# Kernel optimization log

Measured on AMD Instinct MI355X. Metric: run time of the kernel, lower is better.

The kernel has to match this reference:

```python
import jax, jax.numpy as jnp
import numpy as np

NUM_ROUTING_ITER = 3

def _squash(x):
    # Faithful to torch x.norm(): GLOBAL Frobenius norm over the whole tensor.
    n2 = jnp.sum(x * x)
    return x * (jnp.sqrt(n2) / (1.0 + n2))

def setup_inputs() -> dict:
    key = jax.random.key(0)
    k1, k2 = jax.random.split(key)
    x = jax.random.normal(k1, (256, 1152, 8), dtype=jnp.float32)
    weight = jax.random.normal(k2, (10, 1152, 8, 16), dtype=jnp.float32)
    return {"x": x, "weight": weight}

def reference(x, weight):
    # priors: [NC, B, IC, 1, OC] from [1,B,IC,1,L] @ [NC,1,IC,L,OC]
    priors = jnp.einsum('bil,nilo->nbio', x, weight)[:, :, :, None, :]
    b = jnp.zeros_like(priors)
    v = None
    for _ in range(NUM_ROUTING_ITER):
        # legacy F.softmax with no dim on a 5D tensor -> dim=1 (batch dim)
        c = jax.nn.softmax(b, axis=1)
        s = jnp.sum(c * priors, axis=2, keepdims=True)  # [NC,B,1,1,OC]
        v = _squash(s)
        b = b + jnp.sum(priors * v, axis=-1, keepdims=True)
    return v
```

## Files before the change

### kernel.cpp

```cpp
#include <hip/hip_runtime.h>
#include <math.h>

#define NC    10
#define BATCH 256
#define IC    1152
#define LDIM  8
#define OC    16

#define NCH   96
#define CH    (IC/NCH)
#define NBLK  (NC*NCH)
#define NTHR  256
#define NTOT  (NC*BATCH*OC)
#define NRED  160
#define KPG   (NCH/4)

typedef float f32x2 __attribute__((ext_vector_type(2)));

__device__ __forceinline__ int xcd_swizzle(int bid, int nwg) {
    int cpx = nwg >> 3;
    return (bid & 7) * cpx + (bid >> 3);
}

__global__ __launch_bounds__(256) void k0_xT(const float* __restrict__ x,
                                             float* __restrict__ xT)
{
    int u = blockIdx.x * 256 + threadIdx.x;
    int i = u >> 9, r = u & 511, b = r >> 1, h = r & 1;
    reinterpret_cast<float4*>(xT)[u] =
        reinterpret_cast<const float4*>(x)[((size_t)b * IC + i) * 2 + h];
}

__global__ __launch_bounds__(256) void kA(
    const float* __restrict__ xT, const float* __restrict__ w,
    float* __restrict__ s_part)
{
    int wg = xcd_swizzle(blockIdx.x, NBLK);
    int n  = wg / NCH, ch = wg % NCH;
    int i0 = ch * CH;
    int t  = threadIdx.x;

    f32x2 sp2[8];
#pragma unroll
    for (int j = 0; j < 8; ++j) sp2[j] = (f32x2){0.f, 0.f};

    for (int ii = 0; ii < CH; ++ii) {
        int i = i0 + ii;
        const float4* xp = reinterpret_cast<const float4*>(xT)
                         + ((size_t)i * BATCH + t) * 2;
        float4 xa = xp[0], xb = xp[1];
        float xr[8] = {xa.x, xa.y, xa.z, xa.w, xb.x, xb.y, xb.z, xb.w};
        const f32x2* wp2 = reinterpret_cast<const f32x2*>(
            w + (size_t)__builtin_amdgcn_readfirstlane((n * IC + i) * (LDIM * OC)));
#pragma unroll
        for (int l = 0; l < LDIM; ++l) {
            f32x2 xl = {xr[l], xr[l]};
#pragma unroll
            for (int j = 0; j < 8; ++j)
                sp2[j] += wp2[l * 8 + j] * xl;
        }
    }
    float4* dst = reinterpret_cast<float4*>(s_part)
                + (((size_t)ch * NC + n) * BATCH + t) * 4;
    const float inv = 1.0f / 256.0f;
    dst[0] = make_float4(sp2[0].x*inv, sp2[0].y*inv, sp2[1].x*inv, sp2[1].y*inv);
    dst[1] = make_float4(sp2[2].x*inv, sp2[2].y*inv, sp2[3].x*inv, sp2[3].y*inv);
    dst[2] = make_float4(sp2[4].x*inv, sp2[4].y*inv, sp2[5].x*inv, sp2[5].y*inv);
    dst[3] = make_float4(sp2[6].x*inv, sp2[6].y*inv, sp2[7].x*inv, sp2[7].y*inv);
}

__global__ __launch_bounds__(256) void kR(const float* __restrict__ s_part,
                                          float* __restrict__ s,
                                          float* __restrict__ n2_part)
{
    __shared__ float4 lds[4][64];
    int t = threadIdx.x, lane = t & 63, g = t >> 6;
    int idx0 = blockIdx.x * 256;
    const float* base = s_part + idx0 + lane * 4;
    float4 a0 = make_float4(0,0,0,0), a1 = a0, a2 = a0, a3 = a0;
    for (int k = 0; k < KPG; k += 4) {
        float4 v0 = *reinterpret_cast<const float4*>(base + (size_t)(g*KPG + k    ) * NTOT);
        float4 v1 = *reinterpret_cast<const float4*>(base + (size_t)(g*KPG + k + 1) * NTOT);
        float4 v2 = *reinterpret_cast<const float4*>(base + (size_t)(g*KPG + k + 2) * NTOT);
        float4 v3 = *reinterpret_cast<const float4*>(base + (size_t)(g*KPG + k + 3) * NTOT);
        a0.x += v0.x; a0.y += v0.y; a0.z += v0.z; a0.w += v0.w;
        a1.x += v1.x; a1.y += v1.y; a1.z += v1.z; a1.w += v1.w;
        a2.x += v2.x; a2.y += v2.y; a2.z += v2.z; a2.w += v2.w;
        a3.x += v3.x; a3.y += v3.y; a3.z += v3.z; a3.w += v3.w;
    }
    float4 a = make_float4((a0.x+a1.x)+(a2.x+a3.x), (a0.y+a1.y)+(a2.y+a3.y),
                           (a0.z+a1.z)+(a2.z+a3.z), (a0.w+a1.w)+(a2.w+a3.w));
    lds[g][lane] = a;
    __syncthreads();
    if (t < 64) {
        float4 s0 = lds[0][t], s1 = lds[1][t], s2 = lds[2][t], s3 = lds[3][t];
        float4 sv = make_float4((s0.x+s1.x)+(s2.x+s3.x), (s0.y+s1.y)+(s2.y+s3.y),
                                (s0.z+s1.z)+(s2.z+s3.z), (s0.w+s1.w)+(s2.w+s3.w));
        *reinterpret_cast<float4*>(s + idx0 + t * 4) = sv;
        float q = sv.x*sv.x + sv.y*sv.y + sv.z*sv.z + sv.w*sv.w;
#pragma unroll
        for (int m = 32; m >= 1; m >>= 1) q += __shfl_xor(q, m, 64);
        if (t == 0) n2_part[blockIdx.x] = q;
    }
}

template<int MODE>
__global__ __launch_bounds__(256) void kB(
    const float* __restrict__ xT, const float* __restrict__ w,
    const float* __restrict__ s1, const float* __restrict__ n2p1,
    const float* __restrict__ s2, const float* __restrict__ n2p2,
    float* __restrict__ s_part)
{
    __shared__ float redA[2][2][4];
    __shared__ float redW[8];
    int t = threadIdx.x, lane = t & 63, wid = t >> 6;
    int wg = xcd_swizzle(blockIdx.x, NBLK);
    int n  = wg / NCH, ch = wg % NCH;
    int i0 = ch * CH;

    float q1 = (t < NRED) ? n2p1[t] : 0.f;
    float q2 = (MODE == 2 && t < NRED) ? n2p2[t] : 0.f;
#pragma unroll
    for (int m = 32; m >= 1; m >>= 1) {
        q1 += __shfl_xor(q1, m, 64);
        if (MODE == 2) q2 += __shfl_xor(q2, m, 64);
    }
    if (lane == 0) { redW[wid] = q1; redW[4 + wid] = q2; }
    __syncthreads();
    float n2a = (redW[0] + redW[1]) + (redW[2] + redW[3]);
    float sc1 = sqrtf(n2a) / (1.0f + n2a);

    f32x2 v2[8];
    {
        const f32x2* s1p = reinterpret_cast<const f32x2*>(s1)
                         + ((size_t)n * BATCH + t) * 8;
        f32x2 sv = {sc1, sc1};
#pragma unroll
        for (int j = 0; j < 8; ++j) v2[j] = s1p[j] * sv;
        if (MODE == 2) {
            float n2b = (redW[4] + redW[5]) + (redW[6] + redW[7]);
            float sc2 = sqrtf(n2b) / (1.0f + n2b);
            const f32x2* s2p = reinterpret_cast<const f32x2*>(s2)
                             + ((size_t)n * BATCH + t) * 8;
            f32x2 sw = {sc2, sc2};
#pragma unroll
            for (int j = 0; j < 8; ++j) v2[j] += s2p[j] * sw;
        }
    }

    f32x2 sp2[8];
#pragma unroll
    for (int j = 0; j < 8; ++j) sp2[j] = (f32x2){0.f, 0.f};

    for (int pr = 0; pr < CH / 2; ++pr) {
        int i = i0 + 2 * pr;
        const float4* xp = reinterpret_cast<const float4*>(xT)
                         + ((size_t)i * BATCH + t) * 2;
        float4 xa0 = xp[0], xb0 = xp[1];
        float4 xa1 = xp[2 * BATCH], xb1 = xp[2 * BATCH + 1];
        float xr0[8] = {xa0.x, xa0.y, xa0.z, xa0.w, xb0.x, xb0.y, xb0.z, xb0.w};
        float xr1[8] = {xa1.x, xa1.y, xa1.z, xa1.w, xb1.x, xb1.y, xb1.z, xb1.w};
        const f32x2* wp2 = reinterpret_cast<const f32x2*>(
            w + (size_t)__builtin_amdgcn_readfirstlane((n * IC + i) * (LDIM * OC)));

        f32x2 pA[8], pB[8];
#pragma unroll
        for (int j = 0; j < 8; ++j) { pA[j] = (f32x2){0.f,0.f}; pB[j] = (f32x2){0.f,0.f}; }
#pragma unroll
        for (int l = 0; l < LDIM; ++l) {
            f32x2 x0 = {xr0[l], xr0[l]}, x1 = {xr1[l], xr1[l]};
#pragma unroll
            for (int j = 0; j < 8; ++j) {
                pA[j] += wp2[l * 8 + j] * x0;
                pB[j] += wp2[64 + l * 8 + j] * x1;
            }
        }

        f32x2 dA = pA[0] * v2[0], dB = pB[0] * v2[0];
#pragma unroll
        for (int j = 1; j < 8; ++j) { dA += pA[j] * v2[j]; dB += pB[j] * v2[j]; }
        float betaA = dA.x + dA.y, betaB = dB.x + dB.y;

        float eA = __expf(betaA), eB = __expf(betaB);
        float esA = eA, esB = eB;
#pragma unroll
        for (int m = 1; m < 64; m <<= 1) {
            esA += __shfl_xor(esA, m, 64);
            esB += __shfl_xor(esB, m, 64);
        }
        if (lane == 0) { redA[pr & 1][0][wid] = esA; redA[pr & 1][1][wid] = esB; }
        __syncthreads();
        float denA = (redA[pr&1][0][0] + redA[pr&1][0][1])
                   + (redA[pr&1][0][2] + redA[pr&1][0][3]);
        float denB = (redA[pr&1][1][0] + redA[pr&1][1][1])
                   + (redA[pr&1][1][2] + redA[pr&1][1][3]);
        float cA = eA / denA, cB = eB / denB;
        f32x2 cA2 = {cA, cA}, cB2 = {cB, cB};
#pragma unroll
        for (int j = 0; j < 8; ++j) sp2[j] += cA2 * pA[j] + cB2 * pB[j];
    }

    float4* dst = reinterpret_cast<float4*>(s_part)
                + (((size_t)ch * NC + n) * BATCH + t) * 4;
    dst[0] = make_float4(sp2[0].x, sp2[0].y, sp2[1].x, sp2[1].y);
    dst[1] = make_float4(sp2[2].x, sp2[2].y, sp2[3].x, sp2[3].y);
    dst[2] = make_float4(sp2[4].x, sp2[4].y, sp2[5].x, sp2[5].y);
    dst[3] = make_float4(sp2[6].x, sp2[6].y, sp2[7].x, sp2[7].y);
}

__global__ __launch_bounds__(256) void k_out(const float* __restrict__ s,
                                             const float* __restrict__ n2_part,
                                             float* __restrict__ out)
{
    __shared__ float redW[4];
    int t = threadIdx.x, lane = t & 63, wid = t >> 6;
    float q = (t < NRED) ? n2_part[t] : 0.f;
#pragma unroll
    for (int m = 32; m >= 1; m >>= 1) q += __shfl_xor(q, m, 64);
    if (lane == 0) redW[wid] = q;
    __syncthreads();
    float n2 = (redW[0] + redW[1]) + (redW[2] + redW[3]);
    float sc = sqrtf(n2) / (1.0f + n2);
    int idx = blockIdx.x * 256 + t;
    out[idx] = s[idx] * sc;
}

extern "C" void kernel_launch(void* const* d_in, const int* in_sizes, int n_in,
                              void* d_out, int out_size, void* d_ws, size_t ws_size,
                              hipStream_t stream)
{
    const float* x = (const float*)d_in[0];
    const float* w = (const float*)d_in[1];
    float* out = (float*)d_out;
    float* ws  = (float*)d_ws;

    float* xT      = ws;
    float* s_part  = xT + (size_t)IC * BATCH * LDIM;
    float* s1      = s_part + (size_t)NCH * NTOT;
    float* s2      = s1 + NTOT;
    float* s3      = s2 + NTOT;
    float* n2p1    = s3 + NTOT;
    float* n2p2    = n2p1 + NRED;
    float* n2p3    = n2p2 + NRED;

    dim3 blk(256);

    k0_xT<<<2304, blk, 0, stream>>>(x, xT);
    kA<<<NBLK, blk, 0, stream>>>(xT, w, s_part);
    kR<<<NRED, blk, 0, stream>>>(s_part, s1, n2p1);
    kB<1><<<NBLK, blk, 0, stream>>>(xT, w, s1, n2p1, s1, n2p1, s_part);
    kR<<<NRED, blk, 0, stream>>>(s_part, s2, n2p2);
    kB<2><<<NBLK, blk, 0, stream>>>(xT, w, s1, n2p1, s2, n2p2, s_part);
    kR<<<NRED, blk, 0, stream>>>(s_part, s3, n2p3);
    k_out<<<NRED, blk, 0, stream>>>(s3, n2p3, out);
}
```

Measured before the change: 94.28 us.

## Give each wave its own capsules to remove per-pair block barriers in kB

The routing kernel kB used to process input capsules in pairs across the whole 256-thread block, and a block-wide barrier after every pair reduced the batch-softmax denominator. Now each wave owns three input capsules and covers all 256 batch entries with 4 entries per lane. The softmax sum becomes a wave-level shuffle reduction with no __syncthreads. The routing vector v is staged in padded LDS, and the per-wave partial sums are merged with LDS atomics before the store. In exchange it adds about 34KB of LDS, recomputes the priors twice, makes heavy register use (raised via launch_bounds min 3 blocks), and adds LDS atomic contention.

```diff
diff --git a/kernel.cpp b/kernel.cpp
--- a/kernel.cpp
+++ b/kernel.cpp
@@ -14,6 +14,7 @@
 #define NTOT  (NC*BATCH*OC)
 #define NRED  160
 #define KPG   (NCH/4)
+#define VPAD  17
 
 typedef float f32x2 __attribute__((ext_vector_type(2)));
 
@@ -105,13 +106,14 @@
 }
 
 template<int MODE>
-__global__ __launch_bounds__(256) void kB(
+__global__ __launch_bounds__(256, 3) void kB(
     const float* __restrict__ xT, const float* __restrict__ w,
     const float* __restrict__ s1, const float* __restrict__ n2p1,
     const float* __restrict__ s2, const float* __restrict__ n2p2,
     float* __restrict__ s_part)
 {
-    __shared__ float redA[2][2][4];
+    __shared__ float v_lds[BATCH * VPAD];
+    __shared__ float sp_lds[BATCH * VPAD];
     __shared__ float redW[8];
     int t = threadIdx.x, lane = t & 63, wid = t >> 6;
     int wg = xcd_swizzle(blockIdx.x, NBLK);
@@ -130,13 +132,16 @@
     float n2a = (redW[0] + redW[1]) + (redW[2] + redW[3]);
     float sc1 = sqrtf(n2a) / (1.0f + n2a);
 
-    f32x2 v2[8];
     {
         const f32x2* s1p = reinterpret_cast<const f32x2*>(s1)
                          + ((size_t)n * BATCH + t) * 8;
         f32x2 sv = {sc1, sc1};
-#pragma unroll
-        for (int j = 0; j < 8; ++j) v2[j] = s1p[j] * sv;
+        float ve[16];
+#pragma unroll
+        for (int j = 0; j < 8; ++j) {
+            f32x2 a = s1p[j] * sv;
+            ve[2*j] = a.x; ve[2*j+1] = a.y;
+        }
         if (MODE == 2) {
             float n2b = (redW[4] + redW[5]) + (redW[6] + redW[7]);
             float sc2 = sqrtf(n2b) / (1.0f + n2b);
@@ -144,68 +149,97 @@
                              + ((size_t)n * BATCH + t) * 8;
             f32x2 sw = {sc2, sc2};
 #pragma unroll
-            for (int j = 0; j < 8; ++j) v2[j] += s2p[j] * sw;
-        }
-    }
-
-    f32x2 sp2[8];
-#pragma unroll
-    for (int j = 0; j < 8; ++j) sp2[j] = (f32x2){0.f, 0.f};
-
-    for (int pr = 0; pr < CH / 2; ++pr) {
-        int i = i0 + 2 * pr;
-        const float4* xp = reinterpret_cast<const float4*>(xT)
-                         + ((size_t)i * BATCH + t) * 2;
-        float4 xa0 = xp[0], xb0 = xp[1];
-        float4 xa1 = xp[2 * BATCH], xb1 = xp[2 * BATCH + 1];
-        float xr0[8] = {xa0.x, xa0.y, xa0.z, xa0.w, xb0.x, xb0.y, xb0.z, xb0.w};
-        float xr1[8] = {xa1.x, xa1.y, xa1.z, xa1.w, xb1.x, xb1.y, xb1.z, xb1.w};
+            for (int j = 0; j < 8; ++j) {
+                f32x2 a = s2p[j] * sw;
+                ve[2*j] += a.x; ve[2*j+1] += a.y;
+            }
+        }
+#pragma unroll
+        for (int e = 0; e < 16; ++e) v_lds[t * VPAD + e] = ve[e];
+#pragma unroll
+        for (int r = 0; r < VPAD; ++r) sp_lds[t * VPAD + r] = 0.f;
+    }
+    __syncthreads();
+
+    int vb[4];
+#pragma unroll
+    for (int k = 0; k < 4; ++k) vb[k] = (64 * k + lane) * VPAD;
+
+    f32x2 sp[4][8];
+#pragma unroll
+    for (int k = 0; k < 4; ++k)
+#pragma unroll
+        for (int j = 0; j < 8; ++j) sp[k][j] = (f32x2){0.f, 0.f};
+
+    for (int j3 = 0; j3 < 3; ++j3) {
+        int i = i0 + wid * 3 + j3;
+        float xq[4][8];
+#pragma unroll
+        for (int k = 0; k < 4; ++k) {
+            const float4* xp = reinterpret_cast<const float4*>(xT)
+                             + ((size_t)i * BATCH + 64 * k + lane) * 2;
+            float4 xa = xp[0], xb = xp[1];
+            xq[k][0]=xa.x; xq[k][1]=xa.y; xq[k][2]=xa.z; xq[k][3]=xa.w;
+            xq[k][4]=xb.x; xq[k][5]=xb.y; xq[k][6]=xb.z; xq[k][7]=xb.w;
+        }
         const f32x2* wp2 = reinterpret_cast<const f32x2*>(
             w + (size_t)__builtin_amdgcn_readfirstlane((n * IC + i) * (LDIM * OC)));
 
-        f32x2 pA[8], pB[8];
-#pragma unroll
-        for (int j = 0; j < 8; ++j) { pA[j] = (f32x2){0.f,0.f}; pB[j] = (f32x2){0.f,0.f}; }
-#pragma unroll
-        for (int l = 0; l < LDIM; ++l) {
-            f32x2 x0 = {xr0[l], xr0[l]}, x1 = {xr1[l], xr1[l]};
-#pragma unroll
-            for (int j = 0; j < 8; ++j) {
-                pA[j] += wp2[l * 8 + j] * x0;
-                pB[j] += wp2[64 + l * 8 + j] * x1;
+        float e4[4];
+#pragma unroll
+        for (int k = 0; k < 4; ++k) {
+            float dot = 0.f;
+#pragma unroll
+            for (int jj = 0; jj < 8; ++jj) {
+                f32x2 pj = {0.f, 0.f};
+#pragma unroll
+                for (int l = 0; l < LDIM; ++l) {
+                    f32x2 xl = {xq[k][l], xq[k][l]};
+                    pj += wp2[l * 8 + jj] * xl;
+                }
+                dot += pj.x * v_lds[vb[k] + 2*jj] + pj.y * v_lds[vb[k] + 2*jj + 1];
             }
-        }
-
-        f32x2 dA = pA[0] * v2[0], dB = pB[0] * v2[0];
-#pragma unroll
-        for (int j = 1; j < 8; ++j) { dA += pA[j] * v2[j]; dB += pB[j] * v2[j]; }
-        float betaA = dA.x + dA.y, betaB = dB.x + dB.y;
-
-        float eA = __expf(betaA), eB = __expf(betaB);
-        float esA = eA, esB = eB;
-#pragma unroll
-        for (int m = 1; m < 64; m <<= 1) {
-            esA += __shfl_xor(esA, m, 64);
-            esB += __shfl_xor(esB, m, 64);
-        }
-        if (lane == 0) { redA[pr & 1][0][wid] = esA; redA[pr & 1][1][wid] = esB; }
-        __syncthreads();
-        float denA = (redA[pr&1][0][0] + redA[pr&1][0][1])
-                   + (redA[pr&1][0][2] + redA[pr&1][0][3]);
-        float denB = (redA[pr&1][1][0] + redA[pr&1][1][1])
-                   + (redA[pr&1][1][2] + redA[pr&1][1][3]);
-        float cA = eA / denA, cB = eB / denB;
-        f32x2 cA2 = {cA, cA}, cB2 = {cB, cB};
-#pragma unroll
-        for (int j = 0; j < 8; ++j) sp2[j] += cA2 * pA[j] + cB2 * pB[j];
-    }
+            e4[k] = __expf(dot);
+        }
+
+        float esum = (e4[0] + e4[1]) + (e4[2] + e4[3]);
+#pragma unroll
+        for (int m = 1; m < 64; m <<= 1) esum += __shfl_xor(esum, m, 64);
+        float rden = 1.0f / esum;
+
+#pragma unroll
+        for (int k = 0; k < 4; ++k) {
+            float cs = e4[k] * rden;
+            f32x2 ck = {cs, cs};
+#pragma unroll
+            for (int jj = 0; jj < 8; ++jj) {
+                f32x2 pj = {0.f, 0.f};
+#pragma unroll
+                for (int l = 0; l < LDIM; ++l) {
+                    f32x2 xl = {xq[k][l], xq[k][l]};
+                    pj += wp2[l * 8 + jj] * xl;
+                }
+                sp[k][jj] += ck * pj;
+            }
+        }
+    }
+
+#pragma unroll
+    for (int k = 0; k < 4; ++k)
+#pragma unroll
+        for (int jj = 0; jj < 8; ++jj) {
+            atomicAdd(&sp_lds[vb[k] + 2*jj],     sp[k][jj].x);
+            atomicAdd(&sp_lds[vb[k] + 2*jj + 1], sp[k][jj].y);
+        }
+    __syncthreads();
 
     float4* dst = reinterpret_cast<float4*>(s_part)
                 + (((size_t)ch * NC + n) * BATCH + t) * 4;
-    dst[0] = make_float4(sp2[0].x, sp2[0].y, sp2[1].x, sp2[1].y);
-    dst[1] = make_float4(sp2[2].x, sp2[2].y, sp2[3].x, sp2[3].y);
-    dst[2] = make_float4(sp2[4].x, sp2[4].y, sp2[5].x, sp2[5].y);
-    dst[3] = make_float4(sp2[6].x, sp2[6].y, sp2[7].x, sp2[7].y);
+#pragma unroll
+    for (int qd = 0; qd < 4; ++qd) {
+        dst[qd] = make_float4(sp_lds[t*VPAD + 4*qd], sp_lds[t*VPAD + 4*qd + 1],
+                              sp_lds[t*VPAD + 4*qd + 2], sp_lds[t*VPAD + 4*qd + 3]);
+    }
 }
 
 __global__ __launch_bounds__(256) void k_out(const float* __restrict__ s,
```

New measurement: 349.6 us. +270.8%, slower.
